# Performance work log

Hardware: AMD Instinct MI355X
Metric: run time of the kernel (lower is better)

The kernel has to match this reference:

```python
import jax, jax.numpy as jnp
import numpy as np

HEAD_DIM = 128
N_Q_HEADS = 16
N_KV_HEADS = 8
ROPE_THETA = 10000.0


def setup_inputs() -> dict:
    key = jax.random.key(0)
    ks = jax.random.split(key, 5)
    B, S, D, Hq, Hkv = 2, 2048, 4096, 2048, 1024
    sc = 0.02
    hidden_states = jax.random.normal(ks[0], (B, S, D), dtype=jnp.float32)
    wq = jax.random.normal(ks[1], (Hq, D), dtype=jnp.float32) * sc
    wk = jax.random.normal(ks[2], (Hkv, D), dtype=jnp.float32) * sc
    wv = jax.random.normal(ks[3], (Hkv, D), dtype=jnp.float32) * sc
    wo = jax.random.normal(ks[4], (D, Hq), dtype=jnp.float32) * sc
    position_ids = jnp.broadcast_to(jnp.arange(S, dtype=jnp.int64)[None, :], (B, S))
    return {"hidden_states": hidden_states, "position_ids": position_ids,
            "wq": wq, "wk": wk, "wv": wv, "wo": wo}


def _rope_cos_sin(position_ids, dtype):
    # Llama rotary embedding: inv_freq over even dims, emb = cat(freqs, freqs)
    inv_freq = 1.0 / (ROPE_THETA ** (jnp.arange(0, HEAD_DIM, 2, dtype=jnp.float32) / HEAD_DIM))
    freqs = position_ids.astype(jnp.float32)[:, :, None] * inv_freq[None, None, :]  # [B,S,d/2]
    emb = jnp.concatenate([freqs, freqs], axis=-1)  # [B,S,d]
    return jnp.cos(emb).astype(dtype), jnp.sin(emb).astype(dtype)


def _rotate_half(x):
    x1, x2 = jnp.split(x, 2, axis=-1)
    return jnp.concatenate([-x2, x1], axis=-1)


def reference(hidden_states, position_ids, wq, wk, wv, wo):
    B, S, D = hidden_states.shape
    dh = HEAD_DIM
    q = (hidden_states @ wq.T).reshape(B, S, N_Q_HEADS, dh).transpose(0, 2, 1, 3)   # [B,Hq,S,d]
    k = (hidden_states @ wk.T).reshape(B, S, N_KV_HEADS, dh).transpose(0, 2, 1, 3)  # [B,Hkv,S,d]
    v = (hidden_states @ wv.T).reshape(B, S, N_KV_HEADS, dh).transpose(0, 2, 1, 3)

    cos, sin = _rope_cos_sin(position_ids, q.dtype)  # [B,S,d]
    cos, sin = cos[:, None, :, :], sin[:, None, :, :]
    q = q * cos + _rotate_half(q) * sin
    k = k * cos + _rotate_half(k) * sin

    # GQA repeat_interleave(groups, dim=1)
    groups = N_Q_HEADS // N_KV_HEADS
    k = jnp.repeat(k, groups, axis=1)  # [B,Hq,S,d]
    v = jnp.repeat(v, groups, axis=1)

    scale = 1.0 / jnp.sqrt(jnp.asarray(dh, dtype=q.dtype))
    scores = jnp.einsum('bhqd,bhkd->bhqk', q, k) * scale
    causal = jnp.tril(jnp.ones((S, S), dtype=bool))
    scores = jnp.where(causal[None, None, :, :], scores, jnp.finfo(scores.dtype).min)
    probs = jax.nn.softmax(scores, axis=-1)
    attn = jnp.einsum('bhqk,bhkd->bhqd', probs, v)  # [B,Hq,S,d]
    attn = attn.transpose(0, 2, 1, 3).reshape(B, S, N_Q_HEADS * dh)
    return attn @ wo.T
```

## Files before the change

### kernel.cpp

```cpp
#include <hip/hip_runtime.h>
#include <cstdint>
#include <cstddef>

#define B_ 2
#define S_ 2048
#define NQKV 4096
#define HQ 16
#define HKV 8
#define DH 128
#define KOFF 2048
#define VOFF 3072

typedef __attribute__((ext_vector_type(4))) float f32x4;
typedef __attribute__((ext_vector_type(8))) short bf16x8;
typedef __attribute__((ext_vector_type(4))) unsigned int u32x4;
typedef const __attribute__((address_space(1))) void* gas1;
typedef __attribute__((address_space(3))) void* las3;
typedef __attribute__((address_space(3))) char* l3p;

__device__ __forceinline__ ushort f2b(float f) {
  union { float f; unsigned u; } x; x.f = f;
  return (ushort)((x.u + 0x7FFFu + ((x.u >> 16) & 1u)) >> 16);
}
__device__ __forceinline__ float b2f(ushort u) {
  union { unsigned u; float f; } x; x.u = ((unsigned)u) << 16; return x.f;
}

__global__ void prep_cast_kernel(const float4* __restrict__ hs,
                                 const float* __restrict__ wq, const float* __restrict__ wk,
                                 const float* __restrict__ wv,
                                 ushort4* __restrict__ xb, ushort4* __restrict__ wcat) {
  int bid = blockIdx.x;
  if (bid < 16384) {
    int i = bid * 256 + threadIdx.x;
    float4 v = hs[i];
    xb[i] = make_ushort4(f2b(v.x), f2b(v.y), f2b(v.z), f2b(v.w));
  } else {
    int i = (bid - 16384) * 256 + threadIdx.x;
    int row = i >> 10, c4 = i & 1023;
    const float* src = (row < 2048) ? (wq + (size_t)row * 4096)
                     : (row < 3072) ? (wk + (size_t)(row - 2048) * 4096)
                                    : (wv + (size_t)(row - 3072) * 4096);
    float4 v = ((const float4*)src)[c4];
    wcat[i] = make_ushort4(f2b(v.x), f2b(v.y), f2b(v.z), f2b(v.w));
  }
}

#define DSR(dst, addr, off) asm volatile("ds_read_b128 %0, %1 offset:" #off : "=v"(dst) : "v"(addr) : "memory")
#define MFMA16(d, a, b) d = __builtin_amdgcn_mfma_f32_16x16x32_bf16(a, b, d, 0, 0, 0)

template<int OUT_BF16>
__launch_bounds__(512, 2)
__global__ void gemm256(const ushort* __restrict__ A, const ushort* __restrict__ Bm,
                        void* __restrict__ C, int M, int N, int K) {
  __shared__ __attribute__((aligned(16))) char lds[131072];
  const int tid = threadIdx.x;
  const int lane = tid & 63;
  const int w = tid >> 6;
  const int wm = w >> 2, wn = w & 3;
  const int lr = lane & 15, lg = lane >> 4;

  const int nwg = gridDim.x;
  const int cpx = nwg >> 3;
  const int wg = blockIdx.x;
  const int swz = (wg & 7) * cpx + (wg >> 3);
  const int NT = N >> 8;
  const int bm = swz / NT, bn = swz % NT;
  const int m0 = bm * 256, n0 = bn * 256;

  const ushort* Ab = A + (size_t)m0 * K;
  const ushort* Bb = Bm + (size_t)n0 * K;

  const int NKT = K >> 6;

  int srow[2], scol[2];
#pragma unroll
  for (int jj = 0; jj < 2; ++jj) {
    int lb = (jj * 512 + tid) * 16;
    int ls = lb ^ (((lb >> 7) & 7) << 4);
    srow[jj] = ls >> 7;
    scol[jj] = (ls & 127) >> 1;
  }
  const int ldsw = w * 1024;

  auto stage2 = [&](int t, int j) {
    t = (t < NKT - 1) ? t : (NKT - 1);
    const int slot = ((t & 1) << 16) + (j << 14);
    const ushort* src = (j == 1 || j == 2) ? Ab : Bb;
    const int h = (j >= 2) ? 128 : 0;
    const int k0 = t << 6;
#pragma unroll
    for (int jj = 0; jj < 2; ++jj) {
      const ushort* g = src + (size_t)(h + srow[jj]) * K + k0 + scol[jj];
      __builtin_amdgcn_global_load_lds((gas1)(const void*)g,
          (las3)(void*)(lds + slot + jj * 8192 + ldsw), 16, 0, 0);
    }
  };

  const unsigned lds0 = (unsigned)(size_t)(l3p)(void*)lds;
  const int swzc = (lr & 7) << 4;
  const int c0 = (lg * 16) ^ swzc;
  const int c1 = (64 + lg * 16) ^ swzc;
  const unsigned baseA = lds0 + 16384u + wm * 16384u + lr * 128u;
  const unsigned baseB = lds0 + ((wn >> 1) ? 49152u : 0u) + ((wn & 1) * 64 + lr) * 128u;

  f32x4 zero = {0.0f, 0.0f, 0.0f, 0.0f};
  f32x4 acc[8][4];
#pragma unroll
  for (int m = 0; m < 8; ++m)
#pragma unroll
    for (int n = 0; n < 4; ++n) acc[m][n] = zero;

  stage2(0, 0); stage2(0, 1); stage2(0, 2); stage2(0, 3);
  stage2(1, 0); stage2(1, 1);
  asm volatile("s_waitcnt vmcnt(4)" ::: "memory");
  __builtin_amdgcn_s_barrier();

  for (int kt = 0; kt < NKT; ++kt) {
    const unsigned bo = (unsigned)((kt & 1) << 16);
    const unsigned aak0 = baseA + c0 + bo, aak1 = baseA + c1 + bo;
    const unsigned bak0 = baseB + c0 + bo, bak1 = baseB + c1 + bo;

    bf16x8 a0[2][4], a1[2][4], bq[2][2], bq2[2][2];

    DSR(a0[0][0], aak0, 0);    DSR(a0[0][1], aak0, 2048);
    DSR(a0[0][2], aak0, 4096); DSR(a0[0][3], aak0, 6144);
    DSR(a0[1][0], aak1, 0);    DSR(a0[1][1], aak1, 2048);
    DSR(a0[1][2], aak1, 4096); DSR(a0[1][3], aak1, 6144);
    DSR(bq[0][0], bak0, 0);    DSR(bq[0][1], bak0, 2048);
    DSR(bq[1][0], bak1, 0);    DSR(bq[1][1], bak1, 2048);
    stage2(kt + 1, 2);
    asm volatile("s_waitcnt lgkmcnt(8)" ::: "memory");
    __builtin_amdgcn_s_barrier();
    asm volatile("s_waitcnt lgkmcnt(0)" ::: "memory");
    __builtin_amdgcn_sched_barrier(0);
    __builtin_amdgcn_s_setprio(1);
#pragma unroll
    for (int kk = 0; kk < 2; ++kk)
#pragma unroll
      for (int m = 0; m < 4; ++m) {
        MFMA16(acc[m][0], a0[kk][m], bq[kk][0]);
        MFMA16(acc[m][1], a0[kk][m], bq[kk][1]);
      }
    __builtin_amdgcn_s_setprio(0);
    __builtin_amdgcn_s_barrier();

    DSR(bq2[0][0], bak0, 4096); DSR(bq2[0][1], bak0, 6144);
    DSR(bq2[1][0], bak1, 4096); DSR(bq2[1][1], bak1, 6144);
    stage2(kt + 1, 3);
    __builtin_amdgcn_s_barrier();
    asm volatile("s_waitcnt lgkmcnt(0)" ::: "memory");
    __builtin_amdgcn_sched_barrier(0);
    __builtin_amdgcn_s_setprio(1);
#pragma unroll
    for (int kk = 0; kk < 2; ++kk)
#pragma unroll
      for (int m = 0; m < 4; ++m) {
        MFMA16(acc[m][2], a0[kk][m], bq2[kk][0]);
        MFMA16(acc[m][3], a0[kk][m], bq2[kk][1]);
      }
    __builtin_amdgcn_s_setprio(0);
    __builtin_amdgcn_s_barrier();

    DSR(a1[0][0], aak0, 8192);  DSR(a1[0][1], aak0, 10240);
    DSR(a1[0][2], aak0, 12288); DSR(a1[0][3], aak0, 14336);
    DSR(a1[1][0], aak1, 8192);  DSR(a1[1][1], aak1, 10240);
    DSR(a1[1][2], aak1, 12288); DSR(a1[1][3], aak1, 14336);
    stage2(kt + 2, 0);
    __builtin_amdgcn_s_barrier();
    asm volatile("s_waitcnt lgkmcnt(0)" ::: "memory");
    __builtin_amdgcn_sched_barrier(0);
    __builtin_amdgcn_s_setprio(1);
#pragma unroll
    for (int kk = 0; kk < 2; ++kk)
#pragma unroll
      for (int m = 0; m < 4; ++m) {
        MFMA16(acc[m + 4][0], a1[kk][m], bq[kk][0]);
        MFMA16(acc[m + 4][1], a1[kk][m], bq[kk][1]);
      }
    __builtin_amdgcn_s_setprio(0);
    __builtin_amdgcn_s_barrier();

    stage2(kt + 2, 1);
    __builtin_amdgcn_s_barrier();
    __builtin_amdgcn_s_setprio(1);
#pragma unroll
    for (int kk = 0; kk < 2; ++kk)
#pragma unroll
      for (int m = 0; m < 4; ++m) {
        MFMA16(acc[m + 4][2], a1[kk][m], bq2[kk][0]);
        MFMA16(acc[m + 4][3], a1[kk][m], bq2[kk][1]);
      }
    __builtin_amdgcn_s_setprio(0);
    asm volatile("s_waitcnt vmcnt(4)" ::: "memory");
    __builtin_amdgcn_s_barrier();
  }

  asm volatile("s_waitcnt vmcnt(0)" ::: "memory");

#pragma unroll
  for (int m = 0; m < 8; ++m) {
    const int row0 = m0 + wm * 128 + m * 16 + lg * 4;
#pragma unroll
    for (int n = 0; n < 4; ++n) {
      const int col = n0 + wn * 64 + n * 16 + lr;
#pragma unroll
      for (int r = 0; r < 4; ++r) {
        if (OUT_BF16) ((ushort*)C)[(size_t)(row0 + r) * N + col] = f2b(acc[m][n][r]);
        else          ((float*)C)[(size_t)(row0 + r) * N + col] = acc[m][n][r];
      }
    }
  }
}

__global__ void rope_tv_wo_kernel(ushort* __restrict__ qkv, ushort* __restrict__ vt,
                                  const float4* __restrict__ wo, ushort4* __restrict__ wob) {
  __shared__ ushort tile[32][33];
  int bid = blockIdx.x;
  int tid = threadIdx.x;
  if (bid < 24576) {
    int t = bid * 256 + tid;
    int row = t / 1536;
    int idx = t - row * 1536;
    int head = idx >> 6, d = idx & 63;
    int pos = row & (S_ - 1);
    int col = (head < HQ) ? (head * DH + d) : (KOFF + (head - HQ) * DH + d);
    size_t base = (size_t)row * NQKV + col;
    float x1 = b2f(qkv[base]);
    float x2 = b2f(qkv[base + 64]);
    float inv = exp2f((float)d * -0.2076205059304600f);
    float ang = (float)pos * inv;
    float c = cosf(ang), s = sinf(ang);
    qkv[base]      = f2b(x1 * c - x2 * s);
    qkv[base + 64] = f2b(x2 * c + x1 * s);
  } else if (bid < 28672) {
    int b2 = bid - 24576;
    const int s0 = (b2 & 63) * 32, d0 = ((b2 >> 6) & 3) * 32;
    const int bh = b2 >> 8, b = bh >> 3, kvh = bh & 7;
    const int tx = tid & 31, ty = tid >> 5;
    const ushort* src = qkv + (size_t)(b * S_ + s0) * NQKV + VOFF + kvh * DH + d0;
#pragma unroll
    for (int j = 0; j < 32; j += 8)
      tile[ty + j][tx] = src[(size_t)(ty + j) * NQKV + tx];
    __syncthreads();
    ushort* dst = vt + (size_t)((b * HKV + kvh) * DH + d0) * S_ + s0;
#pragma unroll
    for (int j = 0; j < 32; j += 8)
      dst[(size_t)(ty + j) * S_ + tx] = tile[tx][ty + j];
  } else {
    int i = (bid - 28672) * 256 + tid;
    float4 v = wo[i];
    wob[i] = make_ushort4(f2b(v.x), f2b(v.y), f2b(v.z), f2b(v.w));
  }
}

__launch_bounds__(256, 2)
__global__ void attn_kernel(const ushort* __restrict__ qkv, const ushort* __restrict__ vt,
                            ushort* __restrict__ aout) {
  __shared__ ushort Ks[64 * DH];
  __shared__ ushort Vts[DH * 64];
  __shared__ ushort Ps[4][16 * 64];
  __shared__ ushort Es[4][16 * 128];
  const int tid = threadIdx.x, lane = tid & 63, w = tid >> 6;
  const int wg = blockIdx.x;
  const int swz = (wg & 7) * 64 + (wg >> 3);
  const int bh = swz >> 4, qi0 = swz & 15;
  const int b = bh >> 4, h = bh & 15, kvh = h >> 1;
  const int lr = lane & 15, lg = lane >> 4;

  const ushort* Kp = qkv + (size_t)(b * S_) * NQKV + KOFF + kvh * DH;
  const ushort* Vtp = vt + (size_t)(b * HKV + kvh) * DH * S_;
  ushort* Psw = &Ps[w][0];

  int koff[4], kb[4], voff[4], vb[4];
#pragma unroll
  for (int i = 0; i < 4; ++i) {
    int chunk = i * 256 + tid;
    int krow = chunk >> 4, kc = (chunk & 15) * 8;
    koff[i] = krow * NQKV + kc;
    kb[i] = (krow * 256 + kc * 2) ^ ((krow & 7) << 4);
    int vrow = chunk >> 3, vc = (chunk & 7) * 8;
    voff[i] = vrow * S_ + vc;
    vb[i] = (vrow * 128 + vc * 2) ^ ((vrow & 7) << 4);
  }

  f32x4 zero = {0.0f, 0.0f, 0.0f, 0.0f};
  const float SCALE_LOG2E = 0.12751744116470802f;

  for (int pass = 0; pass < 2; ++pass) {
    const int qi = pass ? (31 - qi0) : qi0;
    const int qt0 = qi * 64;
    const int qrow = qt0 + w * 16;
    const int q_lane = qrow + lr;

    bf16x8 qf[4];
    {
      const ushort* Qp = qkv + (size_t)(b * S_ + qrow + lr) * NQKV + h * DH;
#pragma unroll
      for (int ds = 0; ds < 4; ++ds)
        qf[ds] = *(const bf16x8*)(Qp + ds * 32 + lg * 8);
    }

    float m_run = -1e30f, l_run = 0.0f;
    f32x4 acc_o[8];
#pragma unroll
    for (int n = 0; n < 8; ++n) acc_o[n] = zero;

    const int ntiles = qi + 1;
    u32x4 kreg[4], vreg[4];

#pragma unroll
    for (int i = 0; i < 4; ++i) {
      kreg[i] = *(const u32x4*)(Kp + koff[i]);
      vreg[i] = *(const u32x4*)(Vtp + voff[i]);
    }
    __syncthreads();
#pragma unroll
    for (int i = 0; i < 4; ++i) {
      *(u32x4*)((char*)Ks + kb[i]) = kreg[i];
      *(u32x4*)((char*)Vts + vb[i]) = vreg[i];
    }
    __syncthreads();

    for (int t = 0; t < ntiles; ++t) {
      const int kv0 = t * 64;
      if (t + 1 < ntiles) {
        const int kv1 = kv0 + 64;
#pragma unroll
        for (int i = 0; i < 4; ++i) {
          kreg[i] = *(const u32x4*)(Kp + (size_t)kv1 * NQKV + koff[i]);
          vreg[i] = *(const u32x4*)(Vtp + kv1 + voff[i]);
        }
      }

      f32x4 sacc[4];
      __builtin_amdgcn_s_setprio(1);
#pragma unroll
      for (int ct = 0; ct < 4; ++ct) {
        sacc[ct] = zero;
#pragma unroll
        for (int ds = 0; ds < 4; ++ds) {
          int krow = ct * 16 + lr;
          int kbb = (krow * 256 + (ds * 32 + lg * 8) * 2) ^ ((krow & 7) << 4);
          bf16x8 kf = *(const bf16x8*)((const char*)Ks + kbb);
          sacc[ct] = __builtin_amdgcn_mfma_f32_16x16x32_bf16(kf, qf[ds], sacc[ct], 0, 0, 0);
        }
      }
      __builtin_amdgcn_s_setprio(0);

      float sv[4][4];
      float mx = -1e30f;
#pragma unroll
      for (int ct = 0; ct < 4; ++ct)
#pragma unroll
        for (int r = 0; r < 4; ++r) {
          int kv = kv0 + ct * 16 + lg * 4 + r;
          float x = sacc[ct][r] * SCALE_LOG2E;
          sv[ct][r] = (kv <= q_lane) ? x : -1e30f;
          mx = fmaxf(mx, sv[ct][r]);
        }
      mx = fmaxf(mx, __shfl_xor(mx, 16, 64));
      mx = fmaxf(mx, __shfl_xor(mx, 32, 64));
      if (!__all(mx <= m_run + 8.0f)) {
        float mnew = fmaxf(m_run, mx);
        float alpha = __builtin_amdgcn_exp2f(m_run - mnew);
        l_run *= alpha;
#pragma unroll
        for (int n = 0; n < 8; ++n)
#pragma unroll
          for (int r = 0; r < 4; ++r) acc_o[n][r] *= alpha;
        m_run = mnew;
      }
      float psum = 0.0f;
#pragma unroll
      for (int ct = 0; ct < 4; ++ct)
#pragma unroll
        for (int r = 0; r < 4; ++r) {
          float p = __builtin_amdgcn_exp2f(sv[ct][r] - m_run);
          psum += p;
          int kvl = ct * 16 + lg * 4 + r;
          int pb = (lr * 128 + kvl * 2) ^ ((lr & 7) << 4);
          *(ushort*)((char*)Psw + pb) = f2b(p);
        }
      psum += __shfl_xor(psum, 16, 64);
      psum += __shfl_xor(psum, 32, 64);
      l_run += psum;

      asm volatile("s_waitcnt lgkmcnt(0)" ::: "memory");
      __builtin_amdgcn_sched_barrier(0);

      __builtin_amdgcn_s_setprio(1);
#pragma unroll
      for (int ks = 0; ks < 2; ++ks) {
        int pb = (lr * 128 + (ks * 32 + lg * 8) * 2) ^ ((lr & 7) << 4);
        bf16x8 pf = *(const bf16x8*)((const char*)Psw + pb);
#pragma unroll
        for (int n = 0; n < 8; ++n) {
          int vrow = n * 16 + lr;
          int vbb = (vrow * 128 + (ks * 32 + lg * 8) * 2) ^ ((vrow & 7) << 4);
          bf16x8 vf = *(const bf16x8*)((const char*)Vts + vbb);
          acc_o[n] = __builtin_amdgcn_mfma_f32_16x16x32_bf16(vf, pf, acc_o[n], 0, 0, 0);
        }
      }
      __builtin_amdgcn_s_setprio(0);

      if (t + 1 < ntiles) {
        __syncthreads();
#pragma unroll
        for (int i = 0; i < 4; ++i) {
          *(u32x4*)((char*)Ks + kb[i]) = kreg[i];
          *(u32x4*)((char*)Vts + vb[i]) = vreg[i];
        }
        __syncthreads();
      }
    }

    float rl = 1.0f / l_run;
    char* Ew = (char*)&Es[w][0];
#pragma unroll
    for (int n = 0; n < 8; ++n)
#pragma unroll
      for (int rp = 0; rp < 2; ++rp) {
        unsigned lo = f2b(acc_o[n][2 * rp] * rl);
        unsigned hi = f2b(acc_o[n][2 * rp + 1] * rl);
        int d = n * 16 + lg * 4 + 2 * rp;
        int eb = (lr * 256 + d * 2) ^ ((lr & 7) << 4);
        *(unsigned*)(Ew + eb) = lo | (hi << 16);
      }
    ushort* Ap = aout + (size_t)(b * S_ + qrow) * 2048 + h * DH;
#pragma unroll
    for (int it = 0; it < 4; ++it) {
      int c = it * 64 + lane;
      int q = c >> 4, k16 = c & 15;
      int rb = (q * 256 + k16 * 16) ^ ((q & 7) << 4);
      u32x4 v = *(const u32x4*)(Ew + rb);
      *(u32x4*)((char*)(Ap + (size_t)q * 2048) + k16 * 16) = v;
    }
  }
}

extern "C" void kernel_launch(void* const* d_in, const int* in_sizes, int n_in,
                              void* d_out, int out_size, void* d_ws, size_t ws_size,
                              hipStream_t stream) {
  const float* hs = (const float*)d_in[0];
  const float* wq = (const float*)d_in[2];
  const float* wk = (const float*)d_in[3];
  const float* wv = (const float*)d_in[4];
  const float* wo = (const float*)d_in[5];
  char* ws = (char*)d_ws;

  ushort* Xb   = (ushort*)(ws + 0);
  ushort* Wcat = (ushort*)(ws + 33554432);
  ushort* QKV  = (ushort*)(ws + 67108864);
  ushort* Vt   = (ushort*)(ws + 100663296);
  ushort* Wob  = Xb;
  ushort* Aout = Wcat;

  prep_cast_kernel<<<32768, 256, 0, stream>>>((const float4*)hs, wq, wk, wv,
                                              (ushort4*)Xb, (ushort4*)Wcat);
  gemm256<1><<<256, 512, 0, stream>>>(Xb, Wcat, QKV, 4096, 4096, 4096);
  rope_tv_wo_kernel<<<36864, 256, 0, stream>>>(QKV, Vt, (const float4*)wo, (ushort4*)Wob);
  attn_kernel<<<dim3(512), 256, 0, stream>>>(QKV, Vt, Aout);
  gemm256<0><<<256, 512, 0, stream>>>(Aout, Wob, (float*)d_out, 4096, 4096, 2048);
}
```

Measured before the change: 304.8 us.

## Double-buffer K/V tiles in LDS and overlap next QK with softmax/PV

Double-buffers the K and V^T tiles in shared memory. The QK^T MFMAs for tile t+1 now run before the softmax and PV work of tile t, using two alternating score register sets. The global prefetch is moved one tile further ahead. The epilogue staging buffer now aliases the K buffer instead of a separate Es array, which offsets part of the extra LDS. The aim is to hide LDS-write barriers and softmax latency behind MFMA work, at the cost of more registers and LDS, which could reduce occupancy at 2 blocks per CU.

```diff
diff --git a/kernel.cpp b/kernel.cpp
--- a/kernel.cpp
+++ b/kernel.cpp
@@ -257,10 +257,9 @@
 __launch_bounds__(256, 2)
 __global__ void attn_kernel(const ushort* __restrict__ qkv, const ushort* __restrict__ vt,
                             ushort* __restrict__ aout) {
-  __shared__ ushort Ks[64 * DH];
-  __shared__ ushort Vts[DH * 64];
+  __shared__ ushort Ks[2][64 * DH];
+  __shared__ ushort Vts[2][DH * 64];
   __shared__ ushort Ps[4][16 * 64];
-  __shared__ ushort Es[4][16 * 128];
   const int tid = threadIdx.x, lane = tid & 63, w = tid >> 6;
   const int wg = blockIdx.x;
   const int swz = (wg & 7) * 64 + (wg >> 3);
@@ -289,9 +288,9 @@
 
   for (int pass = 0; pass < 2; ++pass) {
     const int qi = pass ? (31 - qi0) : qi0;
-    const int qt0 = qi * 64;
-    const int qrow = qt0 + w * 16;
+    const int qrow = qi * 64 + w * 16;
     const int q_lane = qrow + lr;
+    const int ntiles = qi + 1;
 
     bf16x8 qf[4];
     {
@@ -306,7 +305,6 @@
 #pragma unroll
     for (int n = 0; n < 8; ++n) acc_o[n] = zero;
 
-    const int ntiles = qi + 1;
     u32x4 kreg[4], vreg[4];
 
 #pragma unroll
@@ -322,42 +320,34 @@
     }
     __syncthreads();
 
-    for (int t = 0; t < ntiles; ++t) {
-      const int kv0 = t * 64;
-      if (t + 1 < ntiles) {
-        const int kv1 = kv0 + 64;
-#pragma unroll
-        for (int i = 0; i < 4; ++i) {
-          kreg[i] = *(const u32x4*)(Kp + (size_t)kv1 * NQKV + koff[i]);
-          vreg[i] = *(const u32x4*)(Vtp + kv1 + voff[i]);
-        }
-      }
-
-      f32x4 sacc[4];
+    auto qk_tile = [&](f32x4 (&s)[4], int bufb) {
       __builtin_amdgcn_s_setprio(1);
 #pragma unroll
       for (int ct = 0; ct < 4; ++ct) {
-        sacc[ct] = zero;
+        s[ct] = zero;
 #pragma unroll
         for (int ds = 0; ds < 4; ++ds) {
           int krow = ct * 16 + lr;
           int kbb = (krow * 256 + (ds * 32 + lg * 8) * 2) ^ ((krow & 7) << 4);
-          bf16x8 kf = *(const bf16x8*)((const char*)Ks + kbb);
-          sacc[ct] = __builtin_amdgcn_mfma_f32_16x16x32_bf16(kf, qf[ds], sacc[ct], 0, 0, 0);
+          bf16x8 kf = *(const bf16x8*)((const char*)Ks + bufb + kbb);
+          s[ct] = __builtin_amdgcn_mfma_f32_16x16x32_bf16(kf, qf[ds], s[ct], 0, 0, 0);
         }
       }
       __builtin_amdgcn_s_setprio(0);
-
-      float sv[4][4];
+    };
+
+    auto sm_pv = [&](f32x4 (&s)[4], int t) {
+      const int kv0 = t * 64;
+      const int bufb = (t & 1) << 14;
       float mx = -1e30f;
 #pragma unroll
       for (int ct = 0; ct < 4; ++ct)
 #pragma unroll
         for (int r = 0; r < 4; ++r) {
           int kv = kv0 + ct * 16 + lg * 4 + r;
-          float x = sacc[ct][r] * SCALE_LOG2E;
-          sv[ct][r] = (kv <= q_lane) ? x : -1e30f;
-          mx = fmaxf(mx, sv[ct][r]);
+          float x = s[ct][r] * SCALE_LOG2E;
+          s[ct][r] = (kv <= q_lane) ? x : -1e30f;
+          mx = fmaxf(mx, s[ct][r]);
         }
       mx = fmaxf(mx, __shfl_xor(mx, 16, 64));
       mx = fmaxf(mx, __shfl_xor(mx, 32, 64));
@@ -376,7 +366,7 @@
       for (int ct = 0; ct < 4; ++ct)
 #pragma unroll
         for (int r = 0; r < 4; ++r) {
-          float p = __builtin_amdgcn_exp2f(sv[ct][r] - m_run);
+          float p = __builtin_amdgcn_exp2f(s[ct][r] - m_run);
           psum += p;
           int kvl = ct * 16 + lg * 4 + r;
           int pb = (lr * 128 + kvl * 2) ^ ((lr & 7) << 4);
@@ -398,25 +388,76 @@
         for (int n = 0; n < 8; ++n) {
           int vrow = n * 16 + lr;
           int vbb = (vrow * 128 + (ks * 32 + lg * 8) * 2) ^ ((vrow & 7) << 4);
-          bf16x8 vf = *(const bf16x8*)((const char*)Vts + vbb);
+          bf16x8 vf = *(const bf16x8*)((const char*)Vts + bufb + vbb);
           acc_o[n] = __builtin_amdgcn_mfma_f32_16x16x32_bf16(vf, pf, acc_o[n], 0, 0, 0);
         }
       }
       __builtin_amdgcn_s_setprio(0);
-
+    };
+
+    f32x4 saccA[4], saccB[4];
+    qk_tile(saccA, 0);
+    if (ntiles > 1) {
+#pragma unroll
+      for (int i = 0; i < 4; ++i) {
+        kreg[i] = *(const u32x4*)(Kp + (size_t)64 * NQKV + koff[i]);
+        vreg[i] = *(const u32x4*)(Vtp + 64 + voff[i]);
+      }
+    }
+
+    int t = 0;
+    for (;;) {
       if (t + 1 < ntiles) {
-        __syncthreads();
+        const int wb = ((t + 1) & 1) << 14;
 #pragma unroll
         for (int i = 0; i < 4; ++i) {
-          *(u32x4*)((char*)Ks + kb[i]) = kreg[i];
-          *(u32x4*)((char*)Vts + vb[i]) = vreg[i];
-        }
-        __syncthreads();
-      }
+          *(u32x4*)((char*)Ks + wb + kb[i]) = kreg[i];
+          *(u32x4*)((char*)Vts + wb + vb[i]) = vreg[i];
+        }
+      }
+      __syncthreads();
+      if (t + 1 < ntiles) {
+        qk_tile(saccB, ((t + 1) & 1) << 14);
+        if (t + 2 < ntiles) {
+          const size_t kv2 = (size_t)(t + 2) * 64;
+#pragma unroll
+          for (int i = 0; i < 4; ++i) {
+            kreg[i] = *(const u32x4*)(Kp + kv2 * NQKV + koff[i]);
+            vreg[i] = *(const u32x4*)(Vtp + kv2 + voff[i]);
+          }
+        }
+      }
+      sm_pv(saccA, t);
+      __syncthreads();
+      ++t; if (t >= ntiles) break;
+
+      if (t + 1 < ntiles) {
+        const int wb = ((t + 1) & 1) << 14;
+#pragma unroll
+        for (int i = 0; i < 4; ++i) {
+          *(u32x4*)((char*)Ks + wb + kb[i]) = kreg[i];
+          *(u32x4*)((char*)Vts + wb + vb[i]) = vreg[i];
+        }
+      }
+      __syncthreads();
+      if (t + 1 < ntiles) {
+        qk_tile(saccA, ((t + 1) & 1) << 14);
+        if (t + 2 < ntiles) {
+          const size_t kv2 = (size_t)(t + 2) * 64;
+#pragma unroll
+          for (int i = 0; i < 4; ++i) {
+            kreg[i] = *(const u32x4*)(Kp + kv2 * NQKV + koff[i]);
+            vreg[i] = *(const u32x4*)(Vtp + kv2 + voff[i]);
+          }
+        }
+      }
+      sm_pv(saccB, t);
+      __syncthreads();
+      ++t; if (t >= ntiles) break;
     }
 
     float rl = 1.0f / l_run;
-    char* Ew = (char*)&Es[w][0];
+    char* Ew = (char*)Ks + w * 4096;
 #pragma unroll
     for (int n = 0; n < 8; ++n)
 #pragma unroll
```

Measured after the change: 325.9 us. 1.07x slower.
